# Optimization experiments

Hardware: AMD Instinct MI355X
Metric: run time of the kernel (lower is better)

## Reference

```python
import math
import jax, jax.numpy as jnp
import numpy as np

EPS = 1e-5  # torch LayerNorm default
K_MA = 25   # moving-average kernel


def _layernorm(x, g, b):
    mu = x.mean(-1, keepdims=True)
    var = ((x - mu) ** 2).mean(-1, keepdims=True)
    return (x - mu) * jax.lax.rsqrt(var + EPS) * g + b


def _moving_avg(x, k=K_MA):
    # x: [B, L, C]; edge-replicate pad (k-1)//2 on both sides, avg window k, stride 1
    pad = (k - 1) // 2
    front = jnp.repeat(x[:, :1], pad, axis=1)
    back = jnp.repeat(x[:, -1:], pad, axis=1)
    xp = jnp.concatenate([front, x, back], axis=1)          # [B, L+2*pad, C]
    cs = jnp.cumsum(xp, axis=1)
    cs = jnp.concatenate([jnp.zeros_like(cs[:, :1]), cs], axis=1)
    return (cs[:, k:] - cs[:, :-k]) / k                     # [B, L, C]


def _autocorrelation(q, k, v, factor=1):
    # q,k,v: [B, L, H, D] -> FFT cross-correlation along time, top-k lag aggregation (inference path)
    B, L, H, D = q.shape
    qp = q.transpose(0, 2, 3, 1)                            # [B,H,D,L]
    kp = k.transpose(0, 2, 3, 1)
    vp = v.transpose(0, 2, 3, 1)
    qf = jnp.fft.rfft(qp, axis=-1)
    kf = jnp.fft.rfft(kp, axis=-1)
    corr = jnp.fft.irfft(qf * jnp.conj(kf), n=L, axis=-1)   # [B,H,D,L]

    top_k = int(factor * math.log(L))
    mean_corr = corr.mean(axis=(1, 2))                      # [B,L]
    weights, delay = jax.lax.top_k(mean_corr, top_k)        # [B,k]
    alpha = jax.nn.softmax(weights, axis=-1)                # [B,k]

    base = jnp.arange(L)
    agg = jnp.zeros_like(vp)
    for i in range(top_k):  # small static loop (top_k = 7)
        idx = (base[None, :] + delay[:, i:i + 1]) % L       # circular gather == roll by -delay
        gathered = jnp.take_along_axis(vp, idx[:, None, None, :], axis=-1)
        agg = agg + gathered * alpha[:, i][:, None, None, None]
    return agg.transpose(0, 3, 1, 2)                        # [B,L,H,D]


def _forward(x, Wq, Wk, Wv, Wo, bo, ln_g, ln_b, W1, W2, num_heads=16, factor=1):
    B, L, C = x.shape
    H = num_heads
    D = C // H
    xn = _layernorm(x, ln_g, ln_b)
    q = jnp.einsum('blc,oc->blo', xn, Wq).reshape(B, L, H, D)
    k = jnp.einsum('blc,oc->blo', xn, Wk).reshape(B, L, H, D)
    v = jnp.einsum('blc,oc->blo', xn, Wv).reshape(B, L, H, D)
    agg = _autocorrelation(q, k, v, factor=factor).reshape(B, L, C)
    attn_out = jnp.einsum('blc,oc->blo', agg, Wo) + bo
    x = x + attn_out
    x = x - _moving_avg(x)                                  # decomp1 seasonal part
    # FFN: 1x1 convs == linear layers, exact GELU (torch default)
    y = jax.nn.gelu(jnp.einsum('blc,hc->blh', x, W1), approximate=False)
    y = jnp.einsum('blh,ch->blc', y, W2)
    x = x + y
    x = x - _moving_avg(x)                                  # decomp2 seasonal part
    return x


def setup_inputs() -> dict:
    key = jax.random.key(0)
    ks = jax.random.split(key, 8)
    B, L, C = 8, 2048, 1024
    Hd = 4 * C
    s = 0.02
    return {
        'x': jax.random.normal(ks[0], (B, L, C), dtype=jnp.float32),
        'Wq': jax.random.normal(ks[1], (C, C), dtype=jnp.float32) * s,
        'Wk': jax.random.normal(ks[2], (C, C), dtype=jnp.float32) * s,
        'Wv': jax.random.normal(ks[3], (C, C), dtype=jnp.float32) * s,
        'Wo': jax.random.normal(ks[4], (C, C), dtype=jnp.float32) * s,
        'bo': jnp.zeros((C,), dtype=jnp.float32),
        'ln_g': jnp.ones((C,), dtype=jnp.float32),
        'ln_b': jnp.zeros((C,), dtype=jnp.float32),
        'W1': jax.random.normal(ks[5], (Hd, C), dtype=jnp.float32) * s,
        'W2': jax.random.normal(ks[6], (C, Hd), dtype=jnp.float32) * s,
    }


def reference(x, Wq, Wk, Wv, Wo, bo, ln_g, ln_b, W1, W2):
    return _forward(x, Wq, Wk, Wv, Wo, bo, ln_g, ln_b, W1, W2)
```

## Files before the change

kernel.cpp:

```cpp
#include <hip/hip_runtime.h>
#include <cstdint>
#include <cstddef>


typedef _Float16 half8 __attribute__((ext_vector_type(8)));
typedef _Float16 half4 __attribute__((ext_vector_type(4)));
typedef float floatx4 __attribute__((ext_vector_type(4)));

#define PI_F 3.14159265358979323846f
#define ZP32(i) ((i) + ((i) >> 5))

__device__ __forceinline__ void load_lds16(const void* g, void* l) {
  __builtin_amdgcn_global_load_lds((__attribute__((address_space(1))) void*)g,
                                   (__attribute__((address_space(3))) void*)l,
                                   16, 0, 0);
}

__device__ __forceinline__ float fast_gelu(float v) {
  float u = v * 0.70710678118654752f;
  float au = fabsf(u);
  float t = __builtin_amdgcn_rcpf(1.0f + 0.3275911f * au);
  float poly = t * (0.254829592f +
               t * (-0.284496736f +
               t * (1.421413741f +
               t * (-1.453152027f +
               t * 1.061405429f))));
  float e = __expf(-u * u);
  float erf_abs = 1.0f - poly * e;
  float erfv = copysignf(erf_abs, u);
  return 0.5f * v * (1.0f + erfv);
}


__global__ __launch_bounds__(256) void cvt_f16_kernel(const float* __restrict__ src,
                                                      _Float16* __restrict__ dst, int n4) {
  int i = blockIdx.x * 256 + threadIdx.x;
  if (i >= n4) return;
  float4 v = ((const float4*)src)[i];
  half4 h = {(_Float16)v.x, (_Float16)v.y, (_Float16)v.z, (_Float16)v.w};
  ((half4*)dst)[i] = h;
}

__global__ __launch_bounds__(256) void transpose_f16_kernel(const float* __restrict__ src,
                                                            _Float16* __restrict__ dst, int n) {
  __shared__ float tile[64][65];
  int j0 = blockIdx.y * 64, c0 = blockIdx.x * 64;
  int tr = threadIdx.x >> 4;
  int tc = threadIdx.x & 15;
#pragma unroll
  for (int rr = 0; rr < 64; rr += 16) {
    float4 v = *(const float4*)(src + (size_t)(j0 + tr + rr) * n + c0 + tc * 4);
    tile[tr + rr][tc * 4 + 0] = v.x;
    tile[tr + rr][tc * 4 + 1] = v.y;
    tile[tr + rr][tc * 4 + 2] = v.z;
    tile[tr + rr][tc * 4 + 3] = v.w;
  }
  __syncthreads();
#pragma unroll
  for (int rr = 0; rr < 64; rr += 16) {
    int c = tr + rr;
    half4 h = {(_Float16)tile[tc * 4 + 0][c], (_Float16)tile[tc * 4 + 1][c],
               (_Float16)tile[tc * 4 + 2][c], (_Float16)tile[tc * 4 + 3][c]};
    *(half4*)(dst + (size_t)(c0 + c) * n + j0 + tc * 4) = h;
  }
}

__global__ __launch_bounds__(256) void ln_kernel(const float* __restrict__ x,
                                                 const float* __restrict__ g,
                                                 const float* __restrict__ b,
                                                 _Float16* __restrict__ xn, int C) {
  int row = blockIdx.x;
  int t = threadIdx.x;
  const float4* xr = (const float4*)(x + (size_t)row * C);
  float4 v = xr[t];
  float s = v.x + v.y + v.z + v.w;
  float s2 = v.x * v.x + v.y * v.y + v.z * v.z + v.w * v.w;
  for (int o = 32; o > 0; o >>= 1) {
    s += __shfl_down(s, o, 64);
    s2 += __shfl_down(s2, o, 64);
  }
  __shared__ float red[8];
  int wave = t >> 6, lane = t & 63;
  if (lane == 0) { red[wave] = s; red[4 + wave] = s2; }
  __syncthreads();
  __shared__ float stats[2];
  if (t == 0) {
    float ts = red[0] + red[1] + red[2] + red[3];
    float ts2 = red[4] + red[5] + red[6] + red[7];
    float mu = ts / (float)C;
    float var = ts2 / (float)C - mu * mu;
    stats[0] = mu;
    stats[1] = 1.0f / sqrtf(var + 1e-5f);
  }
  __syncthreads();
  float mu = stats[0], rs = stats[1];
  float4 gv = ((const float4*)g)[t];
  float4 bv = ((const float4*)b)[t];
  half4 h = {(_Float16)((v.x - mu) * rs * gv.x + bv.x),
             (_Float16)((v.y - mu) * rs * gv.y + bv.y),
             (_Float16)((v.z - mu) * rs * gv.z + bv.z),
             (_Float16)((v.w - mu) * rs * gv.w + bv.w)};
  ((half4*)(xn + (size_t)row * C))[t] = h;
}

template <int EPI>
__global__ __launch_bounds__(512, 2) void gemm256_kernel(
    const _Float16* __restrict__ A, const _Float16* __restrict__ Bw,
    int M, int N, int K, int lda, int ldb,
    float* __restrict__ outf, _Float16* __restrict__ outh,
    const float* __restrict__ bias, const float* __restrict__ res,
    const _Float16* __restrict__ resh) {
  __shared__ _Float16 lds[2][2][256 * 64];

  int tid = threadIdx.x;
  int lane = tid & 63;
  int wave = tid >> 6;
  int wm = wave >> 2;
  int wn = wave & 3;
  int ln15 = lane & 15, q4 = lane >> 4;
  int l3 = lane >> 3, l7 = lane & 7;

  int nwg = gridDim.x, orig = blockIdx.x;
  int wg = ((nwg & 7) == 0) ? ((orig & 7) * (nwg >> 3) + (orig >> 3)) : orig;
  int nbn = N >> 8;
  size_t m0 = (size_t)(wg / nbn) << 8;
  size_t n0 = (size_t)(wg % nbn) << 8;

  int sg0 = (q4 ^ l7) << 3;
  int sg1 = ((q4 + 4) ^ l7) << 3;

  floatx4 acc[8][4] = {};

  const _Float16* srcA = A + (m0 + 8 * wave + l3) * (size_t)lda + (size_t)((l7 ^ l3) * 8);
  const _Float16* srcB = Bw + (n0 + 8 * wave + l3) * (size_t)ldb + (size_t)((l7 ^ l3) * 8);
  char* ldsA0 = (char*)&lds[0][0][0] + wave * 1024;
  char* ldsB0 = (char*)&lds[0][1][0] + wave * 1024;

  load_lds16(srcB, ldsB0);
  load_lds16(srcB + (size_t)64 * ldb, ldsB0 + 1 * 8192);
  load_lds16(srcB + (size_t)128 * ldb, ldsB0 + 2 * 8192);
  load_lds16(srcB + (size_t)192 * ldb, ldsB0 + 3 * 8192);
  load_lds16(srcA, ldsA0);
  load_lds16(srcA + (size_t)128 * lda, ldsA0 + 2 * 8192);
  load_lds16(srcA + (size_t)64 * lda, ldsA0 + 1 * 8192);
  load_lds16(srcA + (size_t)192 * lda, ldsA0 + 3 * 8192);
  asm volatile("s_waitcnt vmcnt(2)" ::: "memory");
  __builtin_amdgcn_s_barrier();
  __builtin_amdgcn_sched_barrier(0);

  int nk = K >> 6;
  half8 bf[4][2], aA[2][2];

#define RD_B() _Pragma("unroll") for (int ni = 0; ni < 4; ++ni) {      \
    const _Float16* p_ = cB + ((wn * 64 + ni * 16 + ln15) << 6);       \
    bf[ni][0] = *(const half8*)(p_ + sg0);                             \
    bf[ni][1] = *(const half8*)(p_ + sg1); }
#define RD_A(mi) { const _Float16* p_ = cA + ((wm * 128 + (mi) * 16 + ln15) << 6); \
    aA[(mi) & 1][0] = *(const half8*)(p_ + sg0);                                   \
    aA[(mi) & 1][1] = *(const half8*)(p_ + sg1); }
#define MM(mi) _Pragma("unroll") for (int ni = 0; ni < 4; ++ni) {      \
    acc[mi][ni] = __builtin_amdgcn_mfma_f32_16x16x32_f16(aA[(mi) & 1][0], bf[ni][0], acc[mi][ni], 0, 0, 0); \
    acc[mi][ni] = __builtin_amdgcn_mfma_f32_16x16x32_f16(aA[(mi) & 1][1], bf[ni][1], acc[mi][ni], 0, 0, 0); }

#define PH_MID()                                            \
    __builtin_amdgcn_s_barrier();                           \
    asm volatile("s_waitcnt lgkmcnt(0)" ::: "memory");      \
    __builtin_amdgcn_sched_barrier(0);                      \
    __builtin_amdgcn_s_setprio(1);
#define PH_END()                                            \
    __builtin_amdgcn_s_setprio(0);                          \
    __builtin_amdgcn_s_barrier();                           \
    __builtin_amdgcn_sched_barrier(0);

  for (int t = 0; t < nk; ++t) {
    int cur = t & 1;
    const _Float16* cA = &lds[cur][0][0];
    const _Float16* cB = &lds[cur][1][0];
    const _Float16* As = srcA + (size_t)(t + 1) * 64;
    const _Float16* Bs = srcB + (size_t)(t + 1) * 64;
    char* stA = ldsA0 + (cur ^ 1) * 65536;
    char* stB = ldsB0 + (cur ^ 1) * 65536;
    bool pf = (t + 1 < nk);

    RD_B();
    RD_A(0); RD_A(1);
    if (pf) {
      load_lds16(Bs, stB);
      load_lds16(Bs + (size_t)64 * ldb, stB + 1 * 8192);
      load_lds16(Bs + (size_t)128 * ldb, stB + 2 * 8192);
    }
    PH_MID();
    MM(0); MM(1);
    PH_END();
    RD_A(2); RD_A(3);
    if (pf) {
      load_lds16(Bs + (size_t)192 * ldb, stB + 3 * 8192);
      load_lds16(As, stA);
      load_lds16(As + (size_t)128 * lda, stA + 2 * 8192);
    }
    PH_MID();
    MM(2); MM(3);
    __builtin_amdgcn_s_setprio(0);
    if (pf) {
      asm volatile("s_waitcnt vmcnt(6)" ::: "memory");
    } else {
      asm volatile("s_waitcnt vmcnt(0)" ::: "memory");
    }
    __builtin_amdgcn_s_barrier();
    __builtin_amdgcn_sched_barrier(0);
    RD_A(4); RD_A(5);
    if (pf) {
      load_lds16(As + (size_t)64 * lda, stA + 1 * 8192);
    }
    PH_MID();
    MM(4); MM(5);
    PH_END();
    RD_A(6); RD_A(7);
    if (pf) {
      load_lds16(As + (size_t)192 * lda, stA + 3 * 8192);
    }
    PH_MID();
    MM(6); MM(7);
    __builtin_amdgcn_s_setprio(0);
    asm volatile("s_waitcnt vmcnt(2)" ::: "memory");
    __builtin_amdgcn_s_barrier();
    __builtin_amdgcn_sched_barrier(0);
  }
#undef RD_B
#undef RD_A
#undef MM
#undef PH_MID
#undef PH_END

  if (EPI == 2 || EPI == 7 || EPI == 8 || EPI == 9) {
    _Float16* eb = (_Float16*)&lds[0][0][0];
#pragma unroll
    for (int mi = 0; mi < 8; ++mi) {
#pragma unroll
      for (int ni = 0; ni < 4; ++ni) {
        floatx4 a4 = acc[mi][ni];
        int erow = wm * 128 + mi * 16 + q4 * 4;
        int ecol = wn * 64 + ni * 16 + ln15;
#pragma unroll
        for (int r = 0; r < 4; ++r) {
          float v = a4[r];
          if (EPI == 2) v = fast_gelu(v);
          eb[(size_t)(erow + r) * 256 + ecol] = (_Float16)v;
        }
      }
    }
    __syncthreads();
    int baser = (tid >> 6) * 32 + (((tid & 63) >> 5) << 4);
    int ecol2 = (tid & 31) << 3;
    float4 bv0, bv1;
    if (EPI == 9) {
      bv0 = *(const float4*)(bias + n0 + ecol2);
      bv1 = *(const float4*)(bias + n0 + ecol2 + 4);
    }
#pragma unroll
    for (int jr = 0; jr < 16; ++jr) {
      int row = baser + jr;
      half8 hv = *(const half8*)(eb + (size_t)row * 256 + ecol2);
      size_t gidx = (m0 + row) * (size_t)N + n0 + ecol2;
      if (EPI == 7) {
        half8 pv = *(const half8*)(outh + gidx);
#pragma unroll
        for (int k = 0; k < 8; ++k) hv[k] = (_Float16)((float)hv[k] + (float)pv[k]);
      } else if (EPI == 8) {
        half8 pv = *(const half8*)(resh + gidx);
#pragma unroll
        for (int k = 0; k < 8; ++k) hv[k] = (_Float16)((float)hv[k] + (float)pv[k]);
      } else if (EPI == 9) {
        float4 rv0 = *(const float4*)(res + gidx);
        float4 rv1 = *(const float4*)(res + gidx + 4);
        hv[0] = (_Float16)((float)hv[0] + bv0.x + rv0.x);
        hv[1] = (_Float16)((float)hv[1] + bv0.y + rv0.y);
        hv[2] = (_Float16)((float)hv[2] + bv0.z + rv0.z);
        hv[3] = (_Float16)((float)hv[3] + bv0.w + rv0.w);
        hv[4] = (_Float16)((float)hv[4] + bv1.x + rv1.x);
        hv[5] = (_Float16)((float)hv[5] + bv1.y + rv1.y);
        hv[6] = (_Float16)((float)hv[6] + bv1.z + rv1.z);
        hv[7] = (_Float16)((float)hv[7] + bv1.w + rv1.w);
      }
      *(half8*)(outh + gidx) = hv;
    }
  } else {
#pragma unroll
    for (int mi = 0; mi < 8; ++mi) {
#pragma unroll
      for (int ni = 0; ni < 4; ++ni) {
        floatx4 a4 = acc[mi][ni];
        size_t rowb = m0 + wm * 128 + mi * 16 + q4 * 4;
        size_t col = n0 + wn * 64 + ni * 16 + ln15;
        if (EPI == 5) {
          size_t b = rowb >> 11, l0 = rowb & 2047;
          half4 h = {(_Float16)a4[0], (_Float16)a4[1], (_Float16)a4[2], (_Float16)a4[3]};
          *(half4*)(outh + (((size_t)b * N + col) << 11) + l0) = h;
        } else {
#pragma unroll
          for (int r = 0; r < 4; ++r) {
            size_t idx = (rowb + r) * (size_t)N + col;
            outh[idx] = (_Float16)a4[r];
          }
        }
      }
    }
  }
}


#define CBFLY(ch, ia, ib, wr, wi) {                      \
    float ax_ = z[ch][ia].x, ay_ = z[ch][ia].y;          \
    float bx_ = z[ch][ib].x, by_ = z[ch][ib].y;          \
    float dx_ = ax_ - bx_, dy_ = ay_ - by_;              \
    z[ch][ia].x = ax_ + bx_; z[ch][ia].y = ay_ + by_;    \
    z[ch][ib].x = dx_ * (wr) - dy_ * (wi);               \
    z[ch][ib].y = dx_ * (wi) + dy_ * (wr); }
#define BFLY2(ia, ib, m) { float2 w_ = twl[ZP32(m)];     \
    CBFLY(0, ia, ib, w_.x, w_.y) CBFLY(1, ia, ib, w_.x, w_.y) }

__global__ __launch_bounds__(256) void corr_fft_kernel(const _Float16* __restrict__ F,
                                                       float* __restrict__ S) {
  __shared__ float2 Zs[2][2112];
  __shared__ float2 twl[1056];
  int tid = threadIdx.x;
  int b = blockIdx.x >> 9;
  int c0 = (blockIdx.x & 511) << 1;
  const _Float16* qb = F + ((size_t)(b * 2048 + c0) << 11);
  const _Float16* kb = F + ((size_t)(b * 2048 + 1024 + c0) << 11);

  float2 z[2][8];
#pragma unroll
  for (int j = 0; j < 8; ++j) {
    int p = tid + 256 * j;
    z[0][j] = make_float2((float)qb[p], (float)kb[p]);
    z[1][j] = make_float2((float)qb[2048 + p], (float)kb[2048 + p]);
  }
  for (int m = tid; m < 1024; m += 256) {
    float sn, cs;
    __sincosf(-PI_F * (float)m / 1024.0f, &sn, &cs);
    twl[ZP32(m)] = make_float2(cs, sn);
  }
  __syncthreads();

  BFLY2(0, 4, tid)
  BFLY2(1, 5, tid + 256)
  BFLY2(2, 6, tid + 512)
  BFLY2(3, 7, tid + 768)
  { float2 wA = twl[ZP32(tid << 1)], wB = twl[ZP32((tid + 256) << 1)];
    CBFLY(0, 0, 2, wA.x, wA.y) CBFLY(1, 0, 2, wA.x, wA.y)
    CBFLY(0, 1, 3, wB.x, wB.y) CBFLY(1, 1, 3, wB.x, wB.y)
    CBFLY(0, 4, 6, wA.x, wA.y) CBFLY(1, 4, 6, wA.x, wA.y)
    CBFLY(0, 5, 7, wB.x, wB.y) CBFLY(1, 5, 7, wB.x, wB.y) }
  { float2 wA = twl[ZP32(tid << 2)];
    CBFLY(0, 0, 1, wA.x, wA.y) CBFLY(1, 0, 1, wA.x, wA.y)
    CBFLY(0, 2, 3, wA.x, wA.y) CBFLY(1, 2, 3, wA.x, wA.y)
    CBFLY(0, 4, 5, wA.x, wA.y) CBFLY(1, 4, 5, wA.x, wA.y)
    CBFLY(0, 6, 7, wA.x, wA.y) CBFLY(1, 6, 7, wA.x, wA.y) }

#pragma unroll
  for (int j = 0; j < 8; ++j) {
    int p = tid + 256 * j;
    Zs[0][ZP32(p)] = z[0][j];
    Zs[1][ZP32(p)] = z[1][j];
  }
  __syncthreads();
  int t5 = tid & 31, hi1 = (tid >> 5) << 8;
#pragma unroll
  for (int j = 0; j < 8; ++j) {
    int p = hi1 + t5 + 32 * j;
    z[0][j] = Zs[0][ZP32(p)];
    z[1][j] = Zs[1][ZP32(p)];
  }

  BFLY2(0, 4, t5 << 3)
  BFLY2(1, 5, (t5 + 32) << 3)
  BFLY2(2, 6, (t5 + 64) << 3)
  BFLY2(3, 7, (t5 + 96) << 3)
  { float2 wA = twl[ZP32(t5 << 4)], wB = twl[ZP32((t5 + 32) << 4)];
    CBFLY(0, 0, 2, wA.x, wA.y) CBFLY(1, 0, 2, wA.x, wA.y)
    CBFLY(0, 1, 3, wB.x, wB.y) CBFLY(1, 1, 3, wB.x, wB.y)
    CBFLY(0, 4, 6, wA.x, wA.y) CBFLY(1, 4, 6, wA.x, wA.y)
    CBFLY(0, 5, 7, wB.x, wB.y) CBFLY(1, 5, 7, wB.x, wB.y) }
  { float2 wA = twl[ZP32(t5 << 5)];
    CBFLY(0, 0, 1, wA.x, wA.y) CBFLY(1, 0, 1, wA.x, wA.y)
    CBFLY(0, 2, 3, wA.x, wA.y) CBFLY(1, 2, 3, wA.x, wA.y)
    CBFLY(0, 4, 5, wA.x, wA.y) CBFLY(1, 4, 5, wA.x, wA.y)
    CBFLY(0, 6, 7, wA.x, wA.y) CBFLY(1, 6, 7, wA.x, wA.y) }

#pragma unroll
  for (int j = 0; j < 8; ++j) {
    int p = hi1 + t5 + 32 * j;
    Zs[0][ZP32(p)] = z[0][j];
    Zs[1][ZP32(p)] = z[1][j];
  }
  __syncthreads();
  int t3 = tid & 3, hi2 = (tid >> 2) << 5;
#pragma unroll
  for (int j = 0; j < 8; ++j) {
    int p = hi2 + t3 + 4 * j;
    z[0][j] = Zs[0][ZP32(p)];
    z[1][j] = Zs[1][ZP32(p)];
  }

  BFLY2(0, 4, t3 << 6)
  BFLY2(1, 5, (t3 + 4) << 6)
  BFLY2(2, 6, (t3 + 8) << 6)
  BFLY2(3, 7, (t3 + 12) << 6)
  { float2 wA = twl[ZP32(t3 << 7)], wB = twl[ZP32((t3 + 4) << 7)];
    CBFLY(0, 0, 2, wA.x, wA.y) CBFLY(1, 0, 2, wA.x, wA.y)
    CBFLY(0, 1, 3, wB.x, wB.y) CBFLY(1, 1, 3, wB.x, wB.y)
    CBFLY(0, 4, 6, wA.x, wA.y) CBFLY(1, 4, 6, wA.x, wA.y)
    CBFLY(0, 5, 7, wB.x, wB.y) CBFLY(1, 5, 7, wB.x, wB.y) }
  { float2 wA = twl[ZP32(t3 << 8)];
    CBFLY(0, 0, 1, wA.x, wA.y) CBFLY(1, 0, 1, wA.x, wA.y)
    CBFLY(0, 2, 3, wA.x, wA.y) CBFLY(1, 2, 3, wA.x, wA.y)
    CBFLY(0, 4, 5, wA.x, wA.y) CBFLY(1, 4, 5, wA.x, wA.y)
    CBFLY(0, 6, 7, wA.x, wA.y) CBFLY(1, 6, 7, wA.x, wA.y) }

#pragma unroll
  for (int j = 0; j < 8; ++j) {
    int p = hi2 + t3 + 4 * j;
    Zs[0][ZP32(p)] = z[0][j];
    Zs[1][ZP32(p)] = z[1][j];
  }
  __syncthreads();
#pragma unroll
  for (int j = 0; j < 8; ++j) {
    int p = (tid << 3) + j;
    z[0][j] = Zs[0][ZP32(p)];
    z[1][j] = Zs[1][ZP32(p)];
  }

  CBFLY(0, 0, 2, 1.0f, 0.0f) CBFLY(1, 0, 2, 1.0f, 0.0f)
  CBFLY(0, 1, 3, 0.0f, -1.0f) CBFLY(1, 1, 3, 0.0f, -1.0f)
  CBFLY(0, 4, 6, 1.0f, 0.0f) CBFLY(1, 4, 6, 1.0f, 0.0f)
  CBFLY(0, 5, 7, 0.0f, -1.0f) CBFLY(1, 5, 7, 0.0f, -1.0f)
  CBFLY(0, 0, 1, 1.0f, 0.0f) CBFLY(1, 0, 1, 1.0f, 0.0f)
  CBFLY(0, 2, 3, 1.0f, 0.0f) CBFLY(1, 2, 3, 1.0f, 0.0f)
  CBFLY(0, 4, 5, 1.0f, 0.0f) CBFLY(1, 4, 5, 1.0f, 0.0f)
  CBFLY(0, 6, 7, 1.0f, 0.0f) CBFLY(1, 6, 7, 1.0f, 0.0f)

#pragma unroll
  for (int j = 0; j < 8; ++j) {
    int p = (tid << 3) + j;
    Zs[0][ZP32(p)] = z[0][j];
    Zs[1][ZP32(p)] = z[1][j];
  }
  __syncthreads();
  float* Sb = S + (size_t)blockIdx.x * 2050;
  for (int f = tid; f <= 1024; f += 256) {
    int rf = __brev((unsigned)f) >> 21;
    int rmf = __brev((unsigned)((2048 - f) & 2047)) >> 21;
    float pr = 0.f, pim = 0.f;
#pragma unroll
    for (int ch = 0; ch < 2; ++ch) {
      float2 zf = Zs[ch][ZP32(rf)], zm = Zs[ch][ZP32(rmf)];
      float Qr = 0.5f * (zf.x + zm.x), Qi = 0.5f * (zf.y - zm.y);
      float Kr = 0.5f * (zf.y + zm.y), Ki = -0.5f * (zf.x - zm.x);
      pr += Qr * Kr + Qi * Ki;
      pim += Qi * Kr - Qr * Ki;
    }
    Sb[2 * f] = pr;
    Sb[2 * f + 1] = pim;
  }
}

__global__ __launch_bounds__(256) void spec_reduce_kernel(const float* __restrict__ Sbig,
                                                          float* __restrict__ S8) {
  int f = blockIdx.x * 256 + threadIdx.x;
  int sc = blockIdx.y;
  int b = blockIdx.z;
  if (f >= 2050) return;
  const float* src = Sbig + ((size_t)b * 512 + (size_t)sc * 64) * 2050 + f;
  float s = 0.f;
  for (int i = 0; i < 64; ++i) s += src[(size_t)i * 2050];
  S8[((size_t)b * 8 + sc) * 2050 + f] = s;
}

__global__ __launch_bounds__(256) void corr_topk_kernel(const float* __restrict__ S,
                                                        int* __restrict__ delays,
                                                        float* __restrict__ alphas,
                                                        int C, int L) {
  __shared__ float2 W[2048];
  __shared__ float mc[2048];
  __shared__ float rv[4];
  __shared__ int ri[4];
  __shared__ float swv[7];
  __shared__ int sdi[7];
  int b = blockIdx.x, tid = threadIdx.x;
  const float* Sb = S + (size_t)b * 8 * 2050;
  for (int f = tid; f < 2048; f += 256) {
    int ff = f <= 1024 ? f : 2048 - f;
    float re = 0.f, im = 0.f;
    for (int s = 0; s < 8; ++s) {
      re += Sb[s * 2050 + 2 * ff];
      im += Sb[s * 2050 + 2 * ff + 1];
    }
    W[f] = make_float2(re, f <= 1024 ? -im : im);
  }
  __syncthreads();
  for (int sh = 10; sh >= 0; --sh) {
    int s = 1 << sh;
    for (int j = tid; j < 1024; j += 256) {
      int t = j & (s - 1);
      int i0 = ((j >> sh) << (sh + 1)) | t;
      int i1 = i0 + s;
      float2 a = W[i0], bb = W[i1];
      float ang = -PI_F * (float)t / (float)s;
      float sn, cs;
      __sincosf(ang, &sn, &cs);
      float2 d = make_float2(a.x - bb.x, a.y - bb.y);
      W[i0] = make_float2(a.x + bb.x, a.y + bb.y);
      W[i1] = make_float2(d.x * cs - d.y * sn, d.x * sn + d.y * cs);
    }
    __syncthreads();
  }
  float inv = 1.0f / ((float)C * (float)L);
  for (int t = tid; t < 2048; t += 256) mc[t] = W[__brev((unsigned)t) >> 21].x * inv;
  __syncthreads();
  int wv = tid >> 6, lane = tid & 63;
  for (int it = 0; it < 7; ++it) {
    float bvv = -1e30f;
    int bi = 0;
    for (int e = tid * 8; e < tid * 8 + 8; ++e) {
      float v = mc[e];
      if (v > bvv) { bvv = v; bi = e; }
    }
    for (int o = 32; o > 0; o >>= 1) {
      float ov = __shfl_down(bvv, o, 64);
      int oi = __shfl_down(bi, o, 64);
      if (ov > bvv || (ov == bvv && oi < bi)) { bvv = ov; bi = oi; }
    }
    if (lane == 0) { rv[wv] = bvv; ri[wv] = bi; }
    __syncthreads();
    if (tid == 0) {
      float fv = rv[0];
      int fi = ri[0];
      for (int w2 = 1; w2 < 4; ++w2)
        if (rv[w2] > fv || (rv[w2] == fv && ri[w2] < fi)) { fv = rv[w2]; fi = ri[w2]; }
      swv[it] = fv;
      sdi[it] = fi;
      mc[fi] = -1e30f;
    }
    __syncthreads();
  }
  if (tid == 0) {
    float mx = swv[0];
    for (int i = 1; i < 7; ++i) mx = fmaxf(mx, swv[i]);
    float e[7], s = 0.f;
    for (int i = 0; i < 7; ++i) { e[i] = expf(swv[i] - mx); s += e[i]; }
    for (int i = 0; i < 7; ++i) {
      alphas[b * 7 + i] = e[i] / s;
      delays[b * 7 + i] = sdi[i];
    }
  }
}

__global__ __launch_bounds__(256) void agg_kernel(const _Float16* __restrict__ v,
                                                  const int* __restrict__ delays,
                                                  const float* __restrict__ alphas,
                                                  _Float16* __restrict__ agg,
                                                  int L, int C) {
  int bt = blockIdx.x;
  int b = bt >> 11, t = bt & 2047;
  int tid = threadIdx.x;
  const _Float16* vb = v + (size_t)b * L * C;
  float ax = 0.f, ay = 0.f, az = 0.f, aw = 0.f;
#pragma unroll
  for (int i = 0; i < 7; ++i) {
    int d = delays[b * 7 + i];
    float a = alphas[b * 7 + i];
    int src = t + d;
    if (src >= L) src -= L;
    half4 x = ((const half4*)(vb + (size_t)src * C))[tid];
    ax += a * (float)x.x; ay += a * (float)x.y;
    az += a * (float)x.z; aw += a * (float)x.w;
  }
  half4 h = {(_Float16)ax, (_Float16)ay, (_Float16)az, (_Float16)aw};
  ((half4*)(agg + (size_t)bt * C))[tid] = h;
}

__global__ __launch_bounds__(256) void decomp_hh_kernel(const _Float16* __restrict__ xin,
                                                        _Float16* __restrict__ xout,
                                                        int L, int C) {
  int c = blockIdx.x * 256 + threadIdx.x;
  int t0 = blockIdx.y * 128;
  int b = blockIdx.z;
  const _Float16* xb = xin + (size_t)b * L * C + c;
  float sum = 0.f;
  for (int j = t0 - 12; j <= t0 + 12; ++j) {
    int jc = j < 0 ? 0 : (j > L - 1 ? L - 1 : j);
    sum += (float)xb[(size_t)jc * C];
  }
  for (int t = t0; t < t0 + 128; ++t) {
    float xv = (float)xb[(size_t)t * C];
    float o = xv - sum * (1.0f / 25.0f);
    xout[((size_t)b * L + t) * C + c] = (_Float16)o;
    int nj = t + 13; if (nj > L - 1) nj = L - 1;
    int oj = t - 12; if (oj < 0) oj = 0;
    sum += (float)xb[(size_t)nj * C] - (float)xb[(size_t)oj * C];
  }
}

__global__ __launch_bounds__(256) void decomp_h_kernel(const _Float16* __restrict__ xin,
                                                       float* __restrict__ xout,
                                                       int L, int C) {
  int c = blockIdx.x * 256 + threadIdx.x;
  int t0 = blockIdx.y * 128;
  int b = blockIdx.z;
  const _Float16* xb = xin + (size_t)b * L * C + c;
  float sum = 0.f;
  for (int j = t0 - 12; j <= t0 + 12; ++j) {
    int jc = j < 0 ? 0 : (j > L - 1 ? L - 1 : j);
    sum += (float)xb[(size_t)jc * C];
  }
  for (int t = t0; t < t0 + 128; ++t) {
    float xv = (float)xb[(size_t)t * C];
    float o = xv - sum * (1.0f / 25.0f);
    xout[((size_t)b * L + t) * C + c] = o;
    int nj = t + 13; if (nj > L - 1) nj = L - 1;
    int oj = t - 12; if (oj < 0) oj = 0;
    sum += (float)xb[(size_t)nj * C] - (float)xb[(size_t)oj * C];
  }
}

extern "C" void kernel_launch(void* const* d_in, const int* in_sizes, int n_in,
                              void* d_out, int out_size, void* d_ws, size_t ws_size,
                              hipStream_t stream) {
  const float* x = (const float*)d_in[0];
  const float* Wq = (const float*)d_in[1];
  const float* Wk = (const float*)d_in[2];
  const float* Wv = (const float*)d_in[3];
  const float* Wo = (const float*)d_in[4];
  const float* bo = (const float*)d_in[5];
  const float* lng = (const float*)d_in[6];
  const float* lnb = (const float*)d_in[7];
  const float* W1 = (const float*)d_in[8];
  const float* W2 = (const float*)d_in[9];
  float* out = (float*)d_out;

  const int B = 8, L = 2048, C = 1024, HD = 4096;
  const int M = B * L;

  char* ws = (char*)d_ws;
  size_t off = 0;
  auto alloc = [&](size_t bytes) -> void* {
    void* p = ws + off;
    off = (off + bytes + 255) & ~(size_t)255;
    return p;
  };
  _Float16* wqkh = (_Float16*)alloc((size_t)2 * C * C * 2);
  _Float16* wvoh = (_Float16*)alloc((size_t)C * C * 2);
  _Float16* w1h = (_Float16*)alloc((size_t)HD * C * 2);
  _Float16* w2h = (_Float16*)alloc((size_t)C * HD * 2);
  float* S8 = (float*)alloc((size_t)B * 8 * 2050 * 4);
  int* dl = (int*)alloc(B * 7 * 4);
  float* al = (float*)alloc(B * 7 * 4);
  _Float16* xn = (_Float16*)alloc((size_t)M * C * 2);
  _Float16* qkh = (_Float16*)alloc((size_t)M * 2 * C * 2);
  _Float16* vh = (_Float16*)alloc((size_t)4096 * 2050 * 4);
  (void)ws_size; (void)in_sizes; (void)n_in; (void)out_size;

  _Float16* wvT = vh;
  _Float16* woh = vh + (size_t)C * C;
  float* Sbig = (float*)vh;
  _Float16* aggh = vh;
  _Float16* x1h = qkh;
  _Float16* x2h = xn;
  _Float16* hid2 = qkh;
  _Float16* x3h = vh;

  cvt_f16_kernel<<<(C * C / 4 + 255) / 256, 256, 0, stream>>>(Wq, wqkh, C * C / 4);
  cvt_f16_kernel<<<(C * C / 4 + 255) / 256, 256, 0, stream>>>(Wk, wqkh + (size_t)C * C, C * C / 4);
  cvt_f16_kernel<<<(C * C / 4 + 255) / 256, 256, 0, stream>>>(Wo, woh, C * C / 4);
  transpose_f16_kernel<<<dim3(16, 16), 256, 0, stream>>>(Wv, wvT, C);
  cvt_f16_kernel<<<(HD * C / 4 + 255) / 256, 256, 0, stream>>>(W1, w1h, HD * C / 4);
  cvt_f16_kernel<<<(HD * C / 4 + 255) / 256, 256, 0, stream>>>(W2, w2h, HD * C / 4);
  gemm256_kernel<4><<<16, 512, 0, stream>>>(woh, wvT, C, C, C, C, C,
                                            nullptr, wvoh, nullptr, nullptr, nullptr);
  ln_kernel<<<M, 256, 0, stream>>>(x, lng, lnb, xn, C);
  gemm256_kernel<5><<<(M / 256) * (2 * C / 256), 512, 0, stream>>>(
      xn, wqkh, M, 2 * C, C, C, C, nullptr, qkh, nullptr, nullptr, nullptr);
  corr_fft_kernel<<<B * (C / 2), 256, 0, stream>>>(qkh, Sbig);
  spec_reduce_kernel<<<dim3(9, 8, 8), 256, 0, stream>>>(Sbig, S8);
  corr_topk_kernel<<<B, 256, 0, stream>>>(S8, dl, al, C, L);
  agg_kernel<<<B * L, 256, 0, stream>>>(xn, dl, al, aggh, L, C);
  gemm256_kernel<9><<<(M / 256) * (C / 256), 512, 0, stream>>>(
      aggh, wvoh, M, C, C, C, C, nullptr, x1h, bo, x, nullptr);
  decomp_hh_kernel<<<dim3(C / 256, L / 128, B), 256, 0, stream>>>(x1h, x2h, L, C);
  for (int ci = 0; ci < 2; ++ci) {
    gemm256_kernel<2><<<(M / 256) * (2048 / 256), 512, 0, stream>>>(
        x2h, w1h + (size_t)ci * 2048 * C, M, 2048, C, C, C,
        nullptr, hid2, nullptr, nullptr, nullptr);
    if (ci == 0) {
      gemm256_kernel<8><<<(M / 256) * (C / 256), 512, 0, stream>>>(
          hid2, w2h, M, C, 2048, 2048, HD, nullptr, x3h, nullptr, nullptr, x2h);
    } else {
      gemm256_kernel<7><<<(M / 256) * (C / 256), 512, 0, stream>>>(
          hid2, w2h + 2048, M, C, 2048, 2048, HD, nullptr, x3h, nullptr, nullptr, nullptr);
    }
  }
  decomp_h_kernel<<<dim3(C / 256, L / 128, B), 256, 0, stream>>>(x3h, out, L, C);
}
```

Baseline: 792.2 us.

## Split-K the Wvo weight GEMM, merge FFN down-projection, swizzle epilogue LDS

The 1024x1024 Wo*Wv product now runs as a 4-way split-K over 64 workgroups writing fp32 partials, followed by a small combine kernel. Before, it used only 16 workgroups. The FFN down-projection becomes one K=4096 GEMM that switches its A source halfway, reading hidden halves kept in two buffers (one aliased onto the output). This removes the second GEMM's read-modify-write of x3h. Epilogues now XOR-swizzle LDS staging to reduce bank conflicts, and the QK epilogue transposes through LDS to store contiguous half8 rows. The costs are extra fp32 partial traffic, an added launch, and reuse of the output buffer as scratch.

Result: no change. 789.5 us (-0.3%).

```diff
diff --git a/kernel.cpp b/kernel.cpp
--- a/kernel.cpp
+++ b/kernel.cpp
@@ -65,6 +65,20 @@
   }
 }
 
+__global__ __launch_bounds__(256) void wvo_combine_kernel(const float* __restrict__ p,
+                                                          _Float16* __restrict__ w, int n4) {
+  int i = blockIdx.x * 256 + threadIdx.x;
+  if (i >= n4) return;
+  const size_t S = (size_t)1024 * 1024;
+  float4 a = ((const float4*)p)[i];
+  float4 b = ((const float4*)(p + S))[i];
+  float4 c = ((const float4*)(p + 2 * S))[i];
+  float4 d = ((const float4*)(p + 3 * S))[i];
+  half4 h = {(_Float16)(a.x + b.x + c.x + d.x), (_Float16)(a.y + b.y + c.y + d.y),
+             (_Float16)(a.z + b.z + c.z + d.z), (_Float16)(a.w + b.w + c.w + d.w)};
+  ((half4*)w)[i] = h;
+}
+
 __global__ __launch_bounds__(256) void ln_kernel(const float* __restrict__ x,
                                                  const float* __restrict__ g,
                                                  const float* __restrict__ b,
@@ -109,7 +123,7 @@
     int M, int N, int K, int lda, int ldb,
     float* __restrict__ outf, _Float16* __restrict__ outh,
     const float* __restrict__ bias, const float* __restrict__ res,
-    const _Float16* __restrict__ resh) {
+    const _Float16* __restrict__ resh, const _Float16* __restrict__ Ah2) {
   __shared__ _Float16 lds[2][2][256 * 64];
 
   int tid = threadIdx.x;
@@ -121,7 +135,13 @@
   int l3 = lane >> 3, l7 = lane & 7;
 
   int nwg = gridDim.x, orig = blockIdx.x;
-  int wg = ((nwg & 7) == 0) ? ((orig & 7) * (nwg >> 3) + (orig >> 3)) : orig;
+  int wg, kslice = 0;
+  if (EPI == 10) {
+    kslice = orig >> 4;
+    wg = orig & 15;
+  } else {
+    wg = ((nwg & 7) == 0) ? ((orig & 7) * (nwg >> 3) + (orig >> 3)) : orig;
+  }
   int nbn = N >> 8;
   size_t m0 = (size_t)(wg / nbn) << 8;
   size_t n0 = (size_t)(wg % nbn) << 8;
@@ -131,10 +151,19 @@
 
   floatx4 acc[8][4] = {};
 
-  const _Float16* srcA = A + (m0 + 8 * wave + l3) * (size_t)lda + (size_t)((l7 ^ l3) * 8);
-  const _Float16* srcB = Bw + (n0 + 8 * wave + l3) * (size_t)ldb + (size_t)((l7 ^ l3) * 8);
+  size_t swzoff = (size_t)((l7 ^ l3) * 8);
+  const _Float16* srcA = A + (m0 + 8 * wave + l3) * (size_t)lda + swzoff;
+  const _Float16* srcB = Bw + (n0 + 8 * wave + l3) * (size_t)ldb + swzoff;
+  const _Float16* srcA2 = (Ah2 ? Ah2 : A) + (m0 + 8 * wave + l3) * (size_t)lda + swzoff;
+  if (EPI == 10) {
+    srcA += (size_t)kslice * 256;
+    srcB += (size_t)kslice * 256;
+  }
   char* ldsA0 = (char*)&lds[0][0][0] + wave * 1024;
   char* ldsB0 = (char*)&lds[0][1][0] + wave * 1024;
+
+  int nk = (EPI == 10) ? 4 : (K >> 6);
+  int nswitch = Ah2 ? (nk >> 1) : nk;
 
   load_lds16(srcB, ldsB0);
   load_lds16(srcB + (size_t)64 * ldb, ldsB0 + 1 * 8192);
@@ -148,7 +177,6 @@
   __builtin_amdgcn_s_barrier();
   __builtin_amdgcn_sched_barrier(0);
 
-  int nk = K >> 6;
   half8 bf[4][2], aA[2][2];
 
 #define RD_B() _Pragma("unroll") for (int ni = 0; ni < 4; ++ni) {      \
@@ -176,11 +204,14 @@
     int cur = t & 1;
     const _Float16* cA = &lds[cur][0][0];
     const _Float16* cB = &lds[cur][1][0];
-    const _Float16* As = srcA + (size_t)(t + 1) * 64;
-    const _Float16* Bs = srcB + (size_t)(t + 1) * 64;
+    int tt = t + 1;
+    const _Float16* As;
+    if (Ah2 != nullptr && tt >= nswitch) As = srcA2 + (size_t)(tt - nswitch) * 64;
+    else As = srcA + (size_t)tt * 64;
+    const _Float16* Bs = srcB + (size_t)tt * 64;
     char* stA = ldsA0 + (cur ^ 1) * 65536;
     char* stB = ldsB0 + (cur ^ 1) * 65536;
-    bool pf = (t + 1 < nk);
+    bool pf = (tt < nk);
 
     RD_B();
     RD_A(0); RD_A(1);
@@ -232,20 +263,21 @@
 #undef PH_MID
 #undef PH_END
 
-  if (EPI == 2 || EPI == 7 || EPI == 8 || EPI == 9) {
+  if (EPI == 2 || EPI == 8 || EPI == 9) {
     _Float16* eb = (_Float16*)&lds[0][0][0];
+    int xq = q4 << 4;
 #pragma unroll
     for (int mi = 0; mi < 8; ++mi) {
 #pragma unroll
       for (int ni = 0; ni < 4; ++ni) {
         floatx4 a4 = acc[mi][ni];
         int erow = wm * 128 + mi * 16 + q4 * 4;
-        int ecol = wn * 64 + ni * 16 + ln15;
+        int ecolX = (wn * 64 + ni * 16 + ln15) ^ xq;
 #pragma unroll
         for (int r = 0; r < 4; ++r) {
           float v = a4[r];
           if (EPI == 2) v = fast_gelu(v);
-          eb[(size_t)(erow + r) * 256 + ecol] = (_Float16)v;
+          eb[(size_t)(erow + r) * 256 + ecolX] = (_Float16)v;
         }
       }
     }
@@ -260,13 +292,10 @@
 #pragma unroll
     for (int jr = 0; jr < 16; ++jr) {
       int row = baser + jr;
-      half8 hv = *(const half8*)(eb + (size_t)row * 256 + ecol2);
+      int xr = ((row >> 2) & 3) << 4;
+      half8 hv = *(const half8*)(eb + (size_t)row * 256 + (ecol2 ^ xr));
       size_t gidx = (m0 + row) * (size_t)N + n0 + ecol2;
-      if (EPI == 7) {
-        half8 pv = *(const half8*)(outh + gidx);
-#pragma unroll
-        for (int k = 0; k < 8; ++k) hv[k] = (_Float16)((float)hv[k] + (float)pv[k]);
-      } else if (EPI == 8) {
+      if (EPI == 8) {
         half8 pv = *(const half8*)(resh + gidx);
 #pragma unroll
         for (int k = 0; k < 8; ++k) hv[k] = (_Float16)((float)hv[k] + (float)pv[k]);
@@ -284,6 +313,32 @@
       }
       *(half8*)(outh + gidx) = hv;
     }
+  } else if (EPI == 5) {
+    _Float16* eb = (_Float16*)&lds[0][0][0];
+#pragma unroll
+    for (int mi = 0; mi < 8; ++mi) {
+#pragma unroll
+      for (int ni = 0; ni < 4; ++ni) {
+        floatx4 a4 = acc[mi][ni];
+        int erow = wm * 128 + mi * 16 + q4 * 4;
+        int ecol = wn * 64 + ni * 16 + ln15;
+        int xc = (ecol & 7) << 3;
+#pragma unroll
+        for (int r = 0; r < 4; ++r)
+          eb[(size_t)ecol * 256 + ((erow + r) ^ xc)] = (_Float16)a4[r];
+      }
+    }
+    __syncthreads();
+    size_t bidx = m0 >> 11, l0 = m0 & 2047;
+    int cbase = (tid >> 5) * 16;
+    int l8 = (tid & 31) << 3;
+#pragma unroll
+    for (int jr = 0; jr < 16; ++jr) {
+      int col = cbase + jr;
+      int xc = (col & 7) << 3;
+      half8 hv = *(const half8*)(eb + (size_t)col * 256 + (l8 ^ xc));
+      *(half8*)(outh + ((bidx * N + n0 + col) << 11) + l0 + l8) = hv;
+    }
   } else {
 #pragma unroll
     for (int mi = 0; mi < 8; ++mi) {
@@ -292,17 +347,10 @@
         floatx4 a4 = acc[mi][ni];
         size_t rowb = m0 + wm * 128 + mi * 16 + q4 * 4;
         size_t col = n0 + wn * 64 + ni * 16 + ln15;
-        if (EPI == 5) {
-          size_t b = rowb >> 11, l0 = rowb & 2047;
-          half4 h = {(_Float16)a4[0], (_Float16)a4[1], (_Float16)a4[2], (_Float16)a4[3]};
-          *(half4*)(outh + (((size_t)b * N + col) << 11) + l0) = h;
-        } else {
-#pragma unroll
-          for (int r = 0; r < 4; ++r) {
-            size_t idx = (rowb + r) * (size_t)N + col;
-            outh[idx] = (_Float16)a4[r];
-          }
-        }
+        float* po = outf + (size_t)kslice * M * N;
+#pragma unroll
+        for (int r = 0; r < 4; ++r)
+          po[(rowb + r) * (size_t)N + col] = a4[r];
       }
     }
   }
@@ -664,11 +712,13 @@
 
   _Float16* wvT = vh;
   _Float16* woh = vh + (size_t)C * C;
+  float* wvo32 = (float*)(vh + (size_t)2 * C * C);
   float* Sbig = (float*)vh;
   _Float16* aggh = vh;
   _Float16* x1h = qkh;
   _Float16* x2h = xn;
-  _Float16* hid2 = qkh;
+  _Float16* hidA = qkh;
+  _Float16* hidB = (_Float16*)out;
   _Float16* x3h = vh;
 
   cvt_f16_kernel<<<(C * C / 4 + 255) / 256, 256, 0, stream>>>(Wq, wqkh, C * C / 4);
@@ -677,29 +727,25 @@
   transpose_f16_kernel<<<dim3(16, 16), 256, 0, stream>>>(Wv, wvT, C);
   cvt_f16_kernel<<<(HD * C / 4 + 255) / 256, 256, 0, stream>>>(W1, w1h, HD * C / 4);
   cvt_f16_kernel<<<(HD * C / 4 + 255) / 256, 256, 0, stream>>>(W2, w2h, HD * C / 4);
-  gemm256_kernel<4><<<16, 512, 0, stream>>>(woh, wvT, C, C, C, C, C,
-                                            nullptr, wvoh, nullptr, nullptr, nullptr);
+  gemm256_kernel<10><<<64, 512, 0, stream>>>(woh, wvT, C, C, C, C, C,
+                                             wvo32, nullptr, nullptr, nullptr, nullptr, nullptr);
+  wvo_combine_kernel<<<(C * C / 4 + 255) / 256, 256, 0, stream>>>(wvo32, wvoh, C * C / 4);
   ln_kernel<<<M, 256, 0, stream>>>(x, lng, lnb, xn, C);
   gemm256_kernel<5><<<(M / 256) * (2 * C / 256), 512, 0, stream>>>(
-      xn, wqkh, M, 2 * C, C, C, C, nullptr, qkh, nullptr, nullptr, nullptr);
+      xn, wqkh, M, 2 * C, C, C, C, nullptr, qkh, nullptr, nullptr, nullptr, nullptr);
   corr_fft_kernel<<<B * (C / 2), 256, 0, stream>>>(qkh, Sbig);
   spec_reduce_kernel<<<dim3(9, 8, 8), 256, 0, stream>>>(Sbig, S8);
   corr_topk_kernel<<<B, 256, 0, stream>>>(S8, dl, al, C, L);
   agg_kernel<<<B * L, 256, 0, stream>>>(xn, dl, al, aggh, L, C);
   gemm256_kernel<9><<<(M / 256) * (C / 256), 512, 0, stream>>>(
-      aggh, wvoh, M, C, C, C, C, nullptr, x1h, bo, x, nullptr);
+      aggh, wvoh, M, C, C, C, C, nullptr, x1h, bo, x, nullptr, nullptr);
   decomp_hh_kernel<<<dim3(C / 256, L / 128, B), 256, 0, stream>>>(x1h, x2h, L, C);
-  for (int ci = 0; ci < 2; ++ci) {
-    gemm256_kernel<2><<<(M / 256) * (2048 / 256), 512, 0, stream>>>(
-        x2h, w1h + (size_t)ci * 2048 * C, M, 2048, C, C, C,
-        nullptr, hid2, nullptr, nullptr, nullptr);
-    if (ci == 0) {
-      gemm256_kernel<8><<<(M / 256) * (C / 256), 512, 0, stream>>>(
-          hid2, w2h, M, C, 2048, 2048, HD, nullptr, x3h, nullptr, nullptr, x2h);
-    } else {
-      gemm256_kernel<7><<<(M / 256) * (C / 256), 512, 0, stream>>>(
-          hid2, w2h + 2048, M, C, 2048, 2048, HD, nullptr, x3h, nullptr, nullptr, nullptr);
-    }
-  }
+  gemm256_kernel<2><<<(M / 256) * (2048 / 256), 512, 0, stream>>>(
+      x2h, w1h, M, 2048, C, C, C, nullptr, hidA, nullptr, nullptr, nullptr, nullptr);
+  gemm256_kernel<2><<<(M / 256) * (2048 / 256), 512, 0, stream>>>(
+      x2h, w1h + (size_t)2048 * C, M, 2048, C, C, C,
+      nullptr, hidB, nullptr, nullptr, nullptr, nullptr);
+  gemm256_kernel<8><<<(M / 256) * (C / 256), 512, 0, stream>>>(
+      hidA, w2h, M, C, HD, 2048, HD, nullptr, x3h, nullptr, nullptr, x2h, hidB);
   decomp_h_kernel<<<dim3(C / 256, L / 128, B), 256, 0, stream>>>(x3h, out, L, C);
 }
```
